# Optimization experiments

Measured on AMD Instinct MI355X. Metric: run time of the kernel, lower is better.

The kernel has to match this reference:

```python
import jax, jax.numpy as jnp
import numpy as np

L = 32       # number of labels (groups)
N = 200000   # number of items (cells)
D = 64       # feature channels


def setup_inputs() -> dict:
    key = jax.random.key(0)
    k_lab, k_x = jax.random.split(key)
    # Each item belongs to exactly one label -> binary membership mask [L, N]
    labels = jax.random.randint(k_lab, (N,), 0, L)
    labmap = (jnp.arange(L)[:, None] == labels[None, :]).astype(jnp.float32)  # [L, N]
    X = jax.random.normal(k_x, (D, N), dtype=jnp.float32)  # [D, N]
    return {"labmap": labmap, "X": X}


def reference(labmap, X):
    # Faithful to LabPool.forward with reduction='max':
    #   prd = labmap.unsqueeze(1) * X  -> [L, D, N]
    #   out = prd.max(2)[0].t()        -> [D, L]
    prd = labmap[:, None, :] * X[None, :, :]  # [L, D, N]
    return jnp.max(prd, axis=2).T  # [D, L]
```

## Files before the change

kernel.cpp:

```cpp
#include <hip/hip_runtime.h>


constexpr int L = 32;
constexpr int D = 64;
constexpr int TI = 64;
constexpr int NB = 512;
constexpr int NT = 512;
constexpr int XS_STRIDE = 65;
constexpr int SM_STRIDE = 33;
constexpr int SM_SIZE = D * SM_STRIDE;
constexpr int TBL = D * L;

__global__ __launch_bounds__(NT, 4)
void labpool_main(const float* __restrict__ labmap,
                  const float* __restrict__ X,
                  unsigned* __restrict__ tables, int N, int ntiles)
{
    __shared__ float    Xs[D * XS_STRIDE];
    __shared__ unsigned sm[SM_SIZE];

    const int tid  = threadIdx.x;
    const int wave = tid >> 6;
    const int lane = tid & 63;
    const int item  = lane & 7;
    const int lrow0 = (lane >> 3) << 2;

    unsigned* dst = tables + (size_t)blockIdx.x * TBL;
    if ((int)blockIdx.x >= ntiles) {
        for (int i = tid; i < TBL; i += NT) dst[i] = 0u;
        return;
    }

    for (int i = tid; i < SM_SIZE; i += NT) sm[i] = 0u;

    const int r0 = tid >> 4;
    const int c0 = 4 * (tid & 15);
    const int r1 = r0 + 32;
    const size_t rowOff0 = (size_t)r0 * N + c0;
    const size_t rowOff1 = (size_t)r1 * N + c0;
    const float* mbase = labmap + (size_t)lrow0 * N + wave * 8 + item;

    const int laneX = lane * XS_STRIDE + wave * 8;
    const int laneS = lane * SM_STRIDE;

    auto LOAD = [&](int t, float4& x0, float4& x1, float (&m)[4]) {
        const int n0 = t * TI;
        x0 = *reinterpret_cast<const float4*>(X + rowOff0 + n0);
        x1 = *reinterpret_cast<const float4*>(X + rowOff1 + n0);
        const float* mp = mbase + n0;
        m[0] = mp[0];
        m[1] = mp[(size_t)N];
        m[2] = mp[(size_t)2 * N];
        m[3] = mp[(size_t)3 * N];
    };
    auto STAGE = [&](const float4& x0, const float4& x1) {
        *reinterpret_cast<float4*>(&Xs[r0 * XS_STRIDE + c0]) = x0;
        *reinterpret_cast<float4*>(&Xs[r1 * XS_STRIDE + c0]) = x1;
    };
    auto LABV = [&](const float (&m)[4]) -> unsigned {
        float acc =            (float)(lrow0)     * m[0];
        acc = fmaf((float)(lrow0 + 1), m[1], acc);
        acc = fmaf((float)(lrow0 + 2), m[2], acc);
        acc = fmaf((float)(lrow0 + 3), m[3], acc);
        acc += __shfl_xor(acc, 8);
        acc += __shfl_xor(acc, 16);
        acc += __shfl_xor(acc, 32);
        return (unsigned)acc;
    };
    auto CONSUME = [&](unsigned labv) {
#pragma unroll
        for (int j = 0; j < 8; ++j) {
            const int labj = __builtin_amdgcn_readlane((int)labv, j);
            const float x = Xs[laneX + j];
            atomicMax(&sm[laneS + labj], __float_as_uint(fmaxf(x, 0.f)));
        }
    };

    int t = blockIdx.x;
    float4 xA0, xA1, xB0, xB1;
    float mA[4], mB[4];
    LOAD(t, xA0, xA1, mA);
    if (t + NB < ntiles) LOAD(t + NB, xB0, xB1, mB);

    while (true) {
        STAGE(xA0, xA1);
        const unsigned lvA = LABV(mA);
        __syncthreads();
        if (t + 2 * NB < ntiles) LOAD(t + 2 * NB, xA0, xA1, mA);
        CONSUME(lvA);
        t += NB;
        if (t >= ntiles) break;
        __syncthreads();

        STAGE(xB0, xB1);
        const unsigned lvB = LABV(mB);
        __syncthreads();
        if (t + 2 * NB < ntiles) LOAD(t + 2 * NB, xB0, xB1, mB);
        CONSUME(lvB);
        t += NB;
        if (t >= ntiles) break;
        __syncthreads();
    }

    __syncthreads();
    for (int i = tid; i < TBL; i += NT)
        dst[i] = sm[(i >> 5) * SM_STRIDE + (i & 31)];
}

__global__ __launch_bounds__(256)
void labpool_reduce(const unsigned* __restrict__ tables, float* __restrict__ out, int nb)
{
    __shared__ uint4 red[256];
    const int tid  = threadIdx.x;
    const int d    = blockIdx.x >> 1;
    const int h    = blockIdx.x & 1;
    const int part = tid & 3;
    const int g    = tid >> 2;
    const int base = d * L + h * 16 + part * 4;

    uint4 m = make_uint4(0u, 0u, 0u, 0u);
    for (int b = g; b < nb; b += 64) {
        const uint4 v = *reinterpret_cast<const uint4*>(tables + (size_t)b * TBL + base);
        m.x = (v.x > m.x) ? v.x : m.x;
        m.y = (v.y > m.y) ? v.y : m.y;
        m.z = (v.z > m.z) ? v.z : m.z;
        m.w = (v.w > m.w) ? v.w : m.w;
    }
    red[tid] = m;
    __syncthreads();
#pragma unroll
    for (int s = 128; s >= 4; s >>= 1) {
        if (tid < s) {
            const uint4 v = red[tid + s];
            uint4 r = red[tid];
            r.x = (v.x > r.x) ? v.x : r.x;
            r.y = (v.y > r.y) ? v.y : r.y;
            r.z = (v.z > r.z) ? v.z : r.z;
            r.w = (v.w > r.w) ? v.w : r.w;
            red[tid] = r;
        }
        __syncthreads();
    }
    if (tid < 4) {
        const uint4 r = red[tid];
        float4 f;
        f.x = __uint_as_float(r.x);
        f.y = __uint_as_float(r.y);
        f.z = __uint_as_float(r.z);
        f.w = __uint_as_float(r.w);
        *reinterpret_cast<float4*>(out + d * L + h * 16 + tid * 4) = f;
    }
}

__global__ __launch_bounds__(256)
void labpool_fused_atomic(const float* __restrict__ labmap,
                          const float* __restrict__ X,
                          unsigned* __restrict__ gout, int N)
{
    __shared__ unsigned sm2[D * L];
    __shared__ unsigned char lab[400];
    const int tid = threadIdx.x;
    const int n0 = blockIdx.x * 400;
    for (int i = tid; i < D * L; i += 256) sm2[i] = 0u;
    constexpr int V = 100;
    for (int idx = tid; idx < L * V; idx += 256) {
        const int l = idx / V;
        const int v = idx - l * V;
        const float4 m = *reinterpret_cast<const float4*>(labmap + (size_t)l * N + n0 + 4 * v);
        if (m.x > 0.5f) lab[4 * v + 0] = (unsigned char)l;
        if (m.y > 0.5f) lab[4 * v + 1] = (unsigned char)l;
        if (m.z > 0.5f) lab[4 * v + 2] = (unsigned char)l;
        if (m.w > 0.5f) lab[4 * v + 3] = (unsigned char)l;
    }
    __syncthreads();
    for (int idx = tid; idx < D * V; idx += 256) {
        const int d = idx / V;
        const int v = idx - d * V;
        const float4 x = *reinterpret_cast<const float4*>(X + (size_t)d * N + n0 + 4 * v);
        const uchar4 lv = *reinterpret_cast<const uchar4*>(&lab[4 * v]);
        atomicMax(&sm2[d * L + lv.x], __float_as_uint(fmaxf(x.x, 0.f)));
        atomicMax(&sm2[d * L + lv.y], __float_as_uint(fmaxf(x.y, 0.f)));
        atomicMax(&sm2[d * L + lv.z], __float_as_uint(fmaxf(x.z, 0.f)));
        atomicMax(&sm2[d * L + lv.w], __float_as_uint(fmaxf(x.w, 0.f)));
    }
    __syncthreads();
    for (int i = tid; i < D * L; i += 256) atomicMax(&gout[i], sm2[i]);
}

__global__ void zero_out_k(unsigned* p, int n)
{
    const int i = blockIdx.x * 256 + threadIdx.x;
    if (i < n) p[i] = 0u;
}

extern "C" void kernel_launch(void* const* d_in, const int* in_sizes, int n_in,
                              void* d_out, int out_size, void* d_ws, size_t ws_size,
                              hipStream_t stream)
{
    const float* labmap = (const float*)d_in[0];
    const float* X      = (const float*)d_in[1];
    const int N = in_sizes[0] / L;
    const int ntiles = N / TI;

    const size_t need = (size_t)NB * TBL * sizeof(unsigned);
    if (d_ws && ws_size >= need && (N % TI) == 0) {
        unsigned* tables = (unsigned*)d_ws;
        labpool_main<<<NB, NT, 0, stream>>>(labmap, X, tables, N, ntiles);
        labpool_reduce<<<2 * D, 256, 0, stream>>>(tables, (float*)d_out, NB);
    } else {
        unsigned* gout = (unsigned*)d_out;
        zero_out_k<<<(D * L + 255) / 256, 256, 0, stream>>>(gout, D * L);
        labpool_fused_atomic<<<N / 400, 256, 0, stream>>>(labmap, X, gout, N);
    }
}
```

Before: 22.35 us.

## Double-buffer the X staging tile in LDS to halve barriers per tile

Replaces the single LDS staging buffer with two buffers, so the next tile is staged while the current one is consumed, which removes one __syncthreads per tile. It also cuts live registers by keeping one pair of X float4s instead of two. The cost is doubled LDS use for Xs, which could limit occupancy, and more involved loop control that must handle the tail correctly.

```diff
diff --git a/kernel.cpp b/kernel.cpp
--- a/kernel.cpp
+++ b/kernel.cpp
@@ -16,7 +16,7 @@
                   const float* __restrict__ X,
                   unsigned* __restrict__ tables, int N, int ntiles)
 {
-    __shared__ float    Xs[D * XS_STRIDE];
+    __shared__ float    Xs[2][D * XS_STRIDE];
     __shared__ unsigned sm[SM_SIZE];
 
     const int tid  = threadIdx.x;
@@ -43,19 +43,20 @@
     const int laneX = lane * XS_STRIDE + wave * 8;
     const int laneS = lane * SM_STRIDE;
 
-    auto LOAD = [&](int t, float4& x0, float4& x1, float (&m)[4]) {
+    float4 xr0, xr1;
+    auto LOAD = [&](int t, float (&m)[4]) {
         const int n0 = t * TI;
-        x0 = *reinterpret_cast<const float4*>(X + rowOff0 + n0);
-        x1 = *reinterpret_cast<const float4*>(X + rowOff1 + n0);
+        xr0 = *reinterpret_cast<const float4*>(X + rowOff0 + n0);
+        xr1 = *reinterpret_cast<const float4*>(X + rowOff1 + n0);
         const float* mp = mbase + n0;
         m[0] = mp[0];
         m[1] = mp[(size_t)N];
         m[2] = mp[(size_t)2 * N];
         m[3] = mp[(size_t)3 * N];
     };
-    auto STAGE = [&](const float4& x0, const float4& x1) {
-        *reinterpret_cast<float4*>(&Xs[r0 * XS_STRIDE + c0]) = x0;
-        *reinterpret_cast<float4*>(&Xs[r1 * XS_STRIDE + c0]) = x1;
+    auto STAGE = [&](int b) {
+        *reinterpret_cast<float4*>(&Xs[b][r0 * XS_STRIDE + c0]) = xr0;
+        *reinterpret_cast<float4*>(&Xs[b][r1 * XS_STRIDE + c0]) = xr1;
     };
     auto LABV = [&](const float (&m)[4]) -> unsigned {
         float acc =            (float)(lrow0)     * m[0];
@@ -67,39 +68,42 @@
         acc += __shfl_xor(acc, 32);
         return (unsigned)acc;
     };
-    auto CONSUME = [&](unsigned labv) {
+    auto CONSUME = [&](int b, unsigned labv) {
 #pragma unroll
         for (int j = 0; j < 8; ++j) {
             const int labj = __builtin_amdgcn_readlane((int)labv, j);
-            const float x = Xs[laneX + j];
+            const float x = Xs[b][laneX + j];
             atomicMax(&sm[laneS + labj], __float_as_uint(fmaxf(x, 0.f)));
         }
     };
 
     int t = blockIdx.x;
-    float4 xA0, xA1, xB0, xB1;
     float mA[4], mB[4];
-    LOAD(t, xA0, xA1, mA);
-    if (t + NB < ntiles) LOAD(t + NB, xB0, xB1, mB);
+    LOAD(t, mA);
+    STAGE(0);
+    unsigned lvA = LABV(mA);
+    bool h1 = (t + NB < ntiles);
+    if (h1) LOAD(t + NB, mB);
+    __syncthreads();
 
     while (true) {
-        STAGE(xA0, xA1);
-        const unsigned lvA = LABV(mA);
+        if (h1) STAGE(1);
+        const unsigned lvB = h1 ? LABV(mB) : 0u;
+        if (t + 2 * NB < ntiles) LOAD(t + 2 * NB, mA);
+        CONSUME(0, lvA);
         __syncthreads();
-        if (t + 2 * NB < ntiles) LOAD(t + 2 * NB, xA0, xA1, mA);
-        CONSUME(lvA);
+        if (!h1) break;
         t += NB;
-        if (t >= ntiles) break;
+        h1 = (t + NB < ntiles);
+
+        if (h1) STAGE(0);
+        lvA = h1 ? LABV(mA) : 0u;
+        if (t + 2 * NB < ntiles) LOAD(t + 2 * NB, mB);
+        CONSUME(1, lvB);
         __syncthreads();
-
-        STAGE(xB0, xB1);
-        const unsigned lvB = LABV(mB);
-        __syncthreads();
-        if (t + 2 * NB < ntiles) LOAD(t + 2 * NB, xB0, xB1, mB);
-        CONSUME(lvB);
+        if (!h1) break;
         t += NB;
-        if (t >= ntiles) break;
-        __syncthreads();
+        h1 = (t + NB < ntiles);
     }
 
     __syncthreads();
```

Result: no change. 22.17 us (-0.8%).
